# Kernel optimization log

Measured on AMD Instinct MI355X. Metric: run time of the kernel, lower is better.

The kernel has to match this reference:

```python
import jax, jax.numpy as jnp
import numpy as np

EMB_DIM = 4096
INNER = 1024
VOCAB = 32000
NPRED = 3
B, N = 2, 512
EPS = 1e-6
# weighting constants from MLPSpeculator.__init__
STATE_W = 0.5 ** (0.5 / NPRED)
ALPHA = float(np.sqrt((1.0 - STATE_W ** 2) * (INNER / 2.0)) / STATE_W)  # emb_weight / state_weight


def _ln(x, w, b):
    # LayerNormParameterized with use_mean=False (fms default): RMS-style norm + scale + shift
    x = x * jax.lax.rsqrt(jnp.mean(x * x, axis=-1, keepdims=True) + EPS)
    return x * w + b


def setup_inputs() -> dict:
    key = jax.random.key(0)
    ks = jax.random.split(key, 8)
    s = 1.0 / np.sqrt(INNER)  # reset_parameters init scale
    return {
        "state": jax.random.normal(ks[0], (B, N, EMB_DIM), jnp.float32),
        "inds": jax.random.randint(ks[1], (B, N + NPRED), 0, VOCAB, dtype=jnp.int32),
        "emb_w": jax.random.normal(ks[2], (NPRED, VOCAB, INNER), jnp.float32) * s,
        "proj0_w": jax.random.normal(ks[3], (INNER, EMB_DIM), jnp.float32) * s,
        "proj_w": jax.random.normal(ks[4], (NPRED - 1, INNER, INNER), jnp.float32) * s,
        "head_w": jax.random.normal(ks[5], (NPRED, VOCAB, INNER), jnp.float32) * s,
        "ln_w": jnp.ones((NPRED, INNER), jnp.float32),
        "ln_b": jnp.zeros((NPRED, INNER), jnp.float32),
    }


def reference(state, inds, emb_w, proj0_w, proj_w, head_w, ln_w, ln_b):
    n = state.shape[1]
    outs = []
    for i in range(NPRED):
        z = emb_w[i][inds[:, i:i + n]]                      # [b, n, inner] gather
        W = proj0_w if i == 0 else proj_w[i - 1]            # [inner, emb_dim] or [inner, inner]
        state = jnp.einsum('bnd,id->bni', state, W)
        state = state + ALPHA * z                           # torch.add(..., alpha=emb_w/state_w)
        state = jax.nn.gelu(_ln(state, ln_w[i], ln_b[i]), approximate=False)
        outs.append(jnp.einsum('bni,vi->bnv', state, head_w[i]))  # logits [b, n, vocab]
    return jnp.stack(outs, axis=0)                          # [n_predict, b, n, vocab]
```

## Files before the change

### kernel.cpp

```cpp
#include <hip/hip_runtime.h>
#include <hip/hip_bf16.h>
#include <math.h>

#define EMB_DIM 4096
#define INNER   1024
#define VOCAB   32000
#define NPRED   3
#define SEQ     512
#define TOKENS  1024

typedef __attribute__((ext_vector_type(8))) short bf16x8;
typedef __attribute__((ext_vector_type(4))) float f32x4;

__device__ inline void gload_lds16(const void* g, void* l) {
  __builtin_amdgcn_global_load_lds(
      (const __attribute__((address_space(1))) void*)g,
      (__attribute__((address_space(3))) void*)l, 16, 0, 0);
}

__device__ inline unsigned short f2bf(float f) {
  unsigned u = __float_as_uint(f);
  u += 0x7fffu + ((u >> 16) & 1u);
  return (unsigned short)(u >> 16);
}

__global__ void cvt_kernel(const float4* __restrict__ in, ushort4* __restrict__ out, int n4) {
  int stride = gridDim.x * blockDim.x;
  for (int i = blockIdx.x * blockDim.x + threadIdx.x; i < n4; i += stride) {
    float4 v = in[i];
    ushort4 o;
    o.x = f2bf(v.x); o.y = f2bf(v.y); o.z = f2bf(v.z); o.w = f2bf(v.w);
    out[i] = o;
  }
}

__global__ __launch_bounds__(256) void proj_cvt(const __hip_bfloat16* __restrict__ A,
                                                const __hip_bfloat16* __restrict__ Bw,
                                                float* __restrict__ C, int K,
                                                const float4* __restrict__ cvsrc,
                                                ushort4* __restrict__ cvdst, int n4) {
  if (blockIdx.x >= 64) {
    for (int i = (blockIdx.x - 64) * 256 + threadIdx.x; i < n4; i += 960 * 256) {
      float4 v = cvsrc[i];
      ushort4 o;
      o.x = f2bf(v.x); o.y = f2bf(v.y); o.z = f2bf(v.z); o.w = f2bf(v.w);
      cvdst[i] = o;
    }
    return;
  }
  __shared__ char smem[16384];
  char* As = smem;
  char* Bs = smem + 8192;

  const int tid  = threadIdx.x;
  const int lane = tid & 63;
  const int wave = tid >> 6;
  const int wm = wave >> 1, wn = wave & 1;

  const int bm = (blockIdx.x >> 3) * 128;
  const int bn = (blockIdx.x & 7) * 128;
  const int N = 1024;

  const char* Ag = (const char*)(A  + (size_t)(bm + (tid >> 2)) * K + (tid & 3) * 8);
  const char* Bg = (const char*)(Bw + (size_t)(bn + (tid >> 2)) * K + (tid & 3) * 8);
  const size_t rowskip = (size_t)64 * K * 2;

  f32x4 acc[4][4] = {};

  const int fa = (wm * 64 + (lane & 15)) * 64 + (lane >> 4) * 16;
  const int fb = (wn * 64 + (lane & 15)) * 64 + (lane >> 4) * 16;

  for (int k0 = 0; k0 < K; k0 += 32) {
    gload_lds16(Ag,           As + tid * 16);
    gload_lds16(Ag + rowskip, As + 4096 + tid * 16);
    gload_lds16(Bg,           Bs + tid * 16);
    gload_lds16(Bg + rowskip, Bs + 4096 + tid * 16);
    Ag += 64; Bg += 64;
    __syncthreads();

    bf16x8 af[4], bfv[4];
#pragma unroll
    for (int m = 0; m < 4; ++m) af[m]  = *(const bf16x8*)(As + fa + m * 1024);
#pragma unroll
    for (int n = 0; n < 4; ++n) bfv[n] = *(const bf16x8*)(Bs + fb + n * 1024);
#pragma unroll
    for (int m = 0; m < 4; ++m)
#pragma unroll
      for (int n = 0; n < 4; ++n)
        acc[m][n] = __builtin_amdgcn_mfma_f32_16x16x32_bf16(af[m], bfv[n], acc[m][n], 0, 0, 0);
    __syncthreads();
  }

  const int r0 = bm + wm * 64 + (lane >> 4) * 4;
  const int c0 = bn + wn * 64 + (lane & 15);
#pragma unroll
  for (int m = 0; m < 4; ++m)
#pragma unroll
    for (int n = 0; n < 4; ++n) {
      float* Cp = C + (size_t)(r0 + m * 16) * N + (c0 + n * 16);
#pragma unroll
      for (int r = 0; r < 4; ++r)
        Cp[(size_t)r * N] = acc[m][n][r];
    }
}

__global__ __launch_bounds__(512, 2) void mega(const __hip_bfloat16* __restrict__ A,
                                               const __hip_bfloat16* __restrict__ B,
                                               float* __restrict__ C,
                                               const __hip_bfloat16* __restrict__ Pw,
                                               float* __restrict__ nsf,
                                               const float4* __restrict__ cvsrc,
                                               ushort4* __restrict__ cvdst, int n4,
                                               int mode) {
  __shared__ char smem[131072];
  const int tid  = threadIdx.x;
  const int lane = tid & 63;
  const int wave = tid >> 6;

  if (mode == 0 && blockIdx.x >= 564) {
    for (int i = (blockIdx.x - 564) * 512 + tid; i < n4; i += 460 * 512) {
      float4 v = cvsrc[i];
      ushort4 o;
      o.x = f2bf(v.x); o.y = f2bf(v.y); o.z = f2bf(v.z); o.w = f2bf(v.w);
      cvdst[i] = o;
    }
    return;
  }

  if (mode == 0 && blockIdx.x >= 500) {
    char* As = smem;
    char* Bs = smem + 8192;
    const int p = blockIdx.x - 500;
    const int bm = (p >> 3) * 128;
    const int bn = (p & 7) * 128;
    const int wm = wave >> 2, wn = wave & 3;

    const char* Ag = (const char*)(A  + (size_t)(bm + (tid >> 2)) * INNER + (tid & 3) * 8);
    const char* Bg = (const char*)(Pw + (size_t)(bn + (tid >> 2)) * INNER + (tid & 3) * 8);

    f32x4 acc[4][2] = {};
    const int fa = (wm * 64 + (lane & 15)) * 64 + (lane >> 4) * 16;
    const int fb = (wn * 32 + (lane & 15)) * 64 + (lane >> 4) * 16;

    for (int k0 = 0; k0 < INNER; k0 += 32) {
      gload_lds16(Ag, As + tid * 16);
      gload_lds16(Bg, Bs + tid * 16);
      Ag += 64; Bg += 64;
      __syncthreads();
      bf16x8 af[4], bfv[2];
#pragma unroll
      for (int m = 0; m < 4; ++m) af[m]  = *(const bf16x8*)(As + fa + m * 1024);
#pragma unroll
      for (int n = 0; n < 2; ++n) bfv[n] = *(const bf16x8*)(Bs + fb + n * 1024);
#pragma unroll
      for (int m = 0; m < 4; ++m)
#pragma unroll
        for (int n = 0; n < 2; ++n)
          acc[m][n] = __builtin_amdgcn_mfma_f32_16x16x32_bf16(af[m], bfv[n], acc[m][n], 0, 0, 0);
      __syncthreads();
    }
    const int r0 = bm + wm * 64 + (lane >> 4) * 4;
    const int c0 = bn + wn * 32 + (lane & 15);
#pragma unroll
    for (int m = 0; m < 4; ++m)
#pragma unroll
      for (int n = 0; n < 2; ++n) {
        float* Cp = nsf + (size_t)(r0 + m * 16) * INNER + (c0 + n * 16);
#pragma unroll
        for (int r = 0; r < 4; ++r)
          Cp[(size_t)r * INNER] = acc[m][n][r];
      }
    return;
  }

  const int hid = blockIdx.x;
  const int M = TOKENS, N = VOCAB, K = INNER;
  const int wm = wave >> 2;
  const int wn = wave & 3;

  const int MT = M >> 8;
  const int q = 500 >> 3, r = 500 & 7;
  const int xcd = hid & 7, idx = hid >> 3;
  const int wg = (xcd < r ? xcd * (q + 1) : r * (q + 1) + (xcd - r) * q) + idx;
  const int bm = (wg % MT) * 256;
  const int bn = (wg / MT) * 256;

  f32x4 acc[8][4] = {};

  const int sl   = (lane >> 4) ^ ((lane >> 1) & 3);
  const int aoff = (wm * 128 + (lane & 15)) * 64 + sl * 16;
  const int boff = (wn * 64  + (lane & 15)) * 64 + sl * 16;

#define STAGE_T(PTR, BASEROW, LDSBASE, KT_)                                     \
  {                                                                             \
    _Pragma("unroll")                                                           \
    for (int c = 0; c < 2; ++c) {                                               \
      int chunk = c * 512 + tid;                                                \
      int row = chunk >> 2;                                                     \
      int s = (chunk & 3) ^ ((row >> 1) & 3);                                   \
      gload_lds16(PTR + (size_t)((BASEROW) + row) * K + (KT_) * 32 + s * 8,     \
                  smem + (LDSBASE) + chunk * 16);                               \
    }                                                                           \
  }

  STAGE_T(A, bm, 0,             0)
  STAGE_T(B, bn, 65536,         0)
  STAGE_T(A, bm, 16384,         1)
  STAGE_T(B, bn, 65536 + 16384, 1)
  STAGE_T(A, bm, 32768,         2)
  STAGE_T(B, bn, 65536 + 32768, 2)

  const int KT = K >> 5;
  for (int t = 0; t < KT; ++t) {
    const int bc = (t & 3) * 16384;
    const int bs = ((t + 3) & 3) * 16384;
    const char* Ab = smem + bc;
    const char* Bb = smem + 65536 + bc;

    asm volatile("s_waitcnt vmcnt(8)" ::: "memory");
    __builtin_amdgcn_s_barrier();

    const int pk = (t + 3 < KT) ? t + 3 : KT - 1;

    bf16x8 af0[4], bfv[4];
#pragma unroll
    for (int m = 0; m < 4; ++m) af0[m] = *(const bf16x8*)(Ab + aoff + m * 1024);
#pragma unroll
    for (int n = 0; n < 4; ++n) bfv[n] = *(const bf16x8*)(Bb + boff + n * 1024);
    STAGE_T(A, bm, bs, pk)
    asm volatile("s_waitcnt lgkmcnt(0)" ::: "memory");
    __builtin_amdgcn_sched_barrier(0);
    __builtin_amdgcn_s_setprio(1);
#pragma unroll
    for (int m = 0; m < 4; ++m)
#pragma unroll
      for (int n = 0; n < 4; ++n)
        acc[m][n] = __builtin_amdgcn_mfma_f32_16x16x32_bf16(af0[m], bfv[n], acc[m][n], 0, 0, 0);
    __builtin_amdgcn_s_setprio(0);

    bf16x8 af1[4];
#pragma unroll
    for (int m = 0; m < 4; ++m) af1[m] = *(const bf16x8*)(Ab + aoff + (m + 4) * 1024);
    STAGE_T(B, bn, 65536 + bs, pk)
    asm volatile("s_waitcnt lgkmcnt(0)" ::: "memory");
    __builtin_amdgcn_sched_barrier(0);
    __builtin_amdgcn_s_setprio(1);
#pragma unroll
    for (int m = 0; m < 4; ++m)
#pragma unroll
      for (int n = 0; n < 4; ++n)
        acc[m + 4][n] = __builtin_amdgcn_mfma_f32_16x16x32_bf16(af1[m], bfv[n], acc[m + 4][n], 0, 0, 0);
    __builtin_amdgcn_s_setprio(0);
    __builtin_amdgcn_sched_barrier(0);
  }
  asm volatile("s_waitcnt vmcnt(0)" ::: "memory");

  const int r0 = bm + wm * 128 + (lane >> 4) * 4;
  const int c0 = bn + wn * 64 + (lane & 15);
#pragma unroll
  for (int m = 0; m < 8; ++m)
#pragma unroll
    for (int n = 0; n < 4; ++n) {
      float* Cp = C + (size_t)(r0 + m * 16) * N + (c0 + n * 16);
#pragma unroll
      for (int rr = 0; rr < 4; ++rr)
        Cp[(size_t)rr * N] = acc[m][n][rr];
    }
#undef STAGE_T
}

__global__ __launch_bounds__(256) void fuse_ln_gelu(const float* __restrict__ ns,
    const float* __restrict__ emb,
    const int* __restrict__ inds,
    const float* __restrict__ lnw, const float* __restrict__ lnb,
    ushort4* __restrict__ out_bf16,
    int i, float alpha)
{
  const int t = blockIdx.x;
  const int b = t >> 9, n = t & 511;
  const int idx = inds[b * (SEQ + NPRED) + n + i];

  const float4* x = (const float4*)(ns + (size_t)t * INNER);
  const float4* z = (const float4*)(emb + (size_t)idx * INNER);
  const int j = threadIdx.x;

  float4 xv = x[j], zv = z[j];
  float4 v;
  v.x = xv.x + alpha * zv.x;
  v.y = xv.y + alpha * zv.y;
  v.z = xv.z + alpha * zv.z;
  v.w = xv.w + alpha * zv.w;

  float ss = v.x * v.x + v.y * v.y + v.z * v.z + v.w * v.w;
#pragma unroll
  for (int o = 32; o > 0; o >>= 1) ss += __shfl_down(ss, o);
  __shared__ float red[4];
  if ((threadIdx.x & 63) == 0) red[threadIdx.x >> 6] = ss;
  __syncthreads();
  float total = red[0] + red[1] + red[2] + red[3];
  float r = rsqrtf(total * (1.0f / INNER) + 1e-6f);

  float4 wv = ((const float4*)lnw)[j];
  float4 bv = ((const float4*)lnb)[j];
  const float inv_sqrt2 = 0.70710678118654752f;
  ushort4 o;
  float y;
  y = v.x * r * wv.x + bv.x; o.x = f2bf(0.5f * y * (1.0f + erff(y * inv_sqrt2)));
  y = v.y * r * wv.y + bv.y; o.y = f2bf(0.5f * y * (1.0f + erff(y * inv_sqrt2)));
  y = v.z * r * wv.z + bv.z; o.z = f2bf(0.5f * y * (1.0f + erff(y * inv_sqrt2)));
  y = v.w * r * wv.w + bv.w; o.w = f2bf(0.5f * y * (1.0f + erff(y * inv_sqrt2)));

  out_bf16[(size_t)t * (INNER / 4) + j] = o;
}

extern "C" void kernel_launch(void* const* d_in, const int* in_sizes, int n_in,
                              void* d_out, int out_size, void* d_ws, size_t ws_size,
                              hipStream_t stream) {
  const float* state = (const float*)d_in[0];
  const int*   inds  = (const int*)d_in[1];
  const float* emb_w = (const float*)d_in[2];
  const float* proj0 = (const float*)d_in[3];
  const float* projw = (const float*)d_in[4];
  const float* headw = (const float*)d_in[5];
  const float* lnw   = (const float*)d_in[6];
  const float* lnb   = (const float*)d_in[7];
  float* out = (float*)d_out;

  char* ws = (char*)d_ws;
  __hip_bfloat16* stateA = (__hip_bfloat16*)(ws);
  __hip_bfloat16* stateI = (__hip_bfloat16*)(ws + 8388608);
  float*          nsf    = (float*)        (ws + 10485760);
  __hip_bfloat16* p0b    = (__hip_bfloat16*)(ws + 14680064);
  __hip_bfloat16* pwb    = (__hip_bfloat16*)(ws + 23068672);
  __hip_bfloat16* hb0    = (__hip_bfloat16*)(ws + 27262976);
  __hip_bfloat16* hb1    = (__hip_bfloat16*)(ws + 92798976);

  double sw = pow(0.5, 1.0 / 6.0);
  float alpha = (float)(sqrt((1.0 - sw * sw) * (INNER / 2.0)) / sw);

  auto cvt = [&](const float* src, __hip_bfloat16* dst, size_t n) {
    int n4 = (int)(n / 4);
    int blocks = (n4 + 255) / 256;
    if (blocks > 2048) blocks = 2048;
    cvt_kernel<<<dim3(blocks), dim3(256), 0, stream>>>((const float4*)src, (ushort4*)dst, n4);
  };

  const int hn4 = (int)((size_t)VOCAB * INNER / 4);

  cvt(state, stateA, (size_t)TOKENS * EMB_DIM);
  cvt(proj0, p0b, (size_t)INNER * EMB_DIM);
  cvt(projw, pwb, (size_t)2 * INNER * INNER);

  proj_cvt<<<dim3(1024), dim3(256), 0, stream>>>(stateA, p0b, nsf, EMB_DIM,
      (const float4*)headw, (ushort4*)hb0, hn4);
  fuse_ln_gelu<<<dim3(TOKENS), dim3(256), 0, stream>>>(nsf,
      emb_w, inds, lnw, lnb, (ushort4*)stateI, 0, alpha);

  mega<<<dim3(1024), dim3(512), 0, stream>>>(stateI, hb0, out,
      pwb, nsf,
      (const float4*)(headw + (size_t)1 * VOCAB * INNER), (ushort4*)hb1, hn4, 0);
  fuse_ln_gelu<<<dim3(TOKENS), dim3(256), 0, stream>>>(nsf,
      emb_w + (size_t)1 * VOCAB * INNER, inds,
      lnw + INNER, lnb + INNER, (ushort4*)stateI, 1, alpha);

  mega<<<dim3(1024), dim3(512), 0, stream>>>(stateI, hb1, out + (size_t)TOKENS * VOCAB,
      pwb + (size_t)INNER * INNER, nsf,
      (const float4*)(headw + (size_t)2 * VOCAB * INNER), (ushort4*)hb0, hn4, 0);
  fuse_ln_gelu<<<dim3(TOKENS), dim3(256), 0, stream>>>(nsf,
      emb_w + (size_t)2 * VOCAB * INNER, inds,
      lnw + 2 * INNER, lnb + 2 * INNER, (ushort4*)stateI, 2, alpha);

  mega<<<dim3(500), dim3(512), 0, stream>>>(stateI, hb0, out + (size_t)2 * TOKENS * VOCAB,
      pwb, nsf, (const float4*)headw, (ushort4*)hb1, hn4, 1);
}
```

Baseline: 442.4 us.

## Shrink head GEMM tiles to 256x128 with double buffering for higher occupancy

The vocab-head GEMM tile drops from 256x256 to 256x128, and the 4-stage LDS ring becomes a 2-stage double buffer. LDS falls from 128KB to 48KB, which allows 4 workgroups per CU instead of 2, and the grid doubles to 1000 GEMM blocks. The projection GEMM in proj_cvt also moves to 128x64 tiles with 128 blocks, to spread that work over more CUs. The cost is less data reuse per tile, an extra barrier in each k-iteration, and a shallower prefetch depth, so global-load latency is less hidden.

```diff
diff --git a/kernel.cpp b/kernel.cpp
--- a/kernel.cpp
+++ b/kernel.cpp
@@ -39,8 +39,8 @@
                                                 float* __restrict__ C, int K,
                                                 const float4* __restrict__ cvsrc,
                                                 ushort4* __restrict__ cvdst, int n4) {
-  if (blockIdx.x >= 64) {
-    for (int i = (blockIdx.x - 64) * 256 + threadIdx.x; i < n4; i += 960 * 256) {
+  if (blockIdx.x >= 128) {
+    for (int i = (blockIdx.x - 128) * 256 + threadIdx.x; i < n4; i += 896 * 256) {
       float4 v = cvsrc[i];
       ushort4 o;
       o.x = f2bf(v.x); o.y = f2bf(v.y); o.z = f2bf(v.z); o.w = f2bf(v.w);
@@ -48,7 +48,7 @@
     }
     return;
   }
-  __shared__ char smem[16384];
+  __shared__ char smem[12288];
   char* As = smem;
   char* Bs = smem + 8192;
 
@@ -57,46 +57,45 @@
   const int wave = tid >> 6;
   const int wm = wave >> 1, wn = wave & 1;
 
-  const int bm = (blockIdx.x >> 3) * 128;
-  const int bn = (blockIdx.x & 7) * 128;
+  const int bm = (blockIdx.x >> 4) * 128;
+  const int bn = (blockIdx.x & 15) * 64;
   const int N = 1024;
 
   const char* Ag = (const char*)(A  + (size_t)(bm + (tid >> 2)) * K + (tid & 3) * 8);
   const char* Bg = (const char*)(Bw + (size_t)(bn + (tid >> 2)) * K + (tid & 3) * 8);
-  const size_t rowskip = (size_t)64 * K * 2;
-
-  f32x4 acc[4][4] = {};
+  const size_t rowskipA = (size_t)64 * K * 2;
+
+  f32x4 acc[4][2] = {};
 
   const int fa = (wm * 64 + (lane & 15)) * 64 + (lane >> 4) * 16;
-  const int fb = (wn * 64 + (lane & 15)) * 64 + (lane >> 4) * 16;
+  const int fb = (wn * 32 + (lane & 15)) * 64 + (lane >> 4) * 16;
 
   for (int k0 = 0; k0 < K; k0 += 32) {
-    gload_lds16(Ag,           As + tid * 16);
-    gload_lds16(Ag + rowskip, As + 4096 + tid * 16);
-    gload_lds16(Bg,           Bs + tid * 16);
-    gload_lds16(Bg + rowskip, Bs + 4096 + tid * 16);
+    gload_lds16(Ag,            As + tid * 16);
+    gload_lds16(Ag + rowskipA, As + 4096 + tid * 16);
+    gload_lds16(Bg,            Bs + tid * 16);
     Ag += 64; Bg += 64;
     __syncthreads();
 
-    bf16x8 af[4], bfv[4];
+    bf16x8 af[4], bfv[2];
 #pragma unroll
     for (int m = 0; m < 4; ++m) af[m]  = *(const bf16x8*)(As + fa + m * 1024);
 #pragma unroll
-    for (int n = 0; n < 4; ++n) bfv[n] = *(const bf16x8*)(Bs + fb + n * 1024);
+    for (int n = 0; n < 2; ++n) bfv[n] = *(const bf16x8*)(Bs + fb + n * 1024);
 #pragma unroll
     for (int m = 0; m < 4; ++m)
 #pragma unroll
-      for (int n = 0; n < 4; ++n)
+      for (int n = 0; n < 2; ++n)
         acc[m][n] = __builtin_amdgcn_mfma_f32_16x16x32_bf16(af[m], bfv[n], acc[m][n], 0, 0, 0);
     __syncthreads();
   }
 
   const int r0 = bm + wm * 64 + (lane >> 4) * 4;
-  const int c0 = bn + wn * 64 + (lane & 15);
+  const int c0 = bn + wn * 32 + (lane & 15);
 #pragma unroll
   for (int m = 0; m < 4; ++m)
 #pragma unroll
-    for (int n = 0; n < 4; ++n) {
+    for (int n = 0; n < 2; ++n) {
       float* Cp = C + (size_t)(r0 + m * 16) * N + (c0 + n * 16);
 #pragma unroll
       for (int r = 0; r < 4; ++r)
@@ -104,7 +103,7 @@
     }
 }
 
-__global__ __launch_bounds__(512, 2) void mega(const __hip_bfloat16* __restrict__ A,
+__global__ __launch_bounds__(512, 4) void mega(const __hip_bfloat16* __restrict__ A,
                                                const __hip_bfloat16* __restrict__ B,
                                                float* __restrict__ C,
                                                const __hip_bfloat16* __restrict__ Pw,
@@ -112,13 +111,13 @@
                                                const float4* __restrict__ cvsrc,
                                                ushort4* __restrict__ cvdst, int n4,
                                                int mode) {
-  __shared__ char smem[131072];
+  __shared__ char smem[49152];
   const int tid  = threadIdx.x;
   const int lane = tid & 63;
   const int wave = tid >> 6;
 
-  if (mode == 0 && blockIdx.x >= 564) {
-    for (int i = (blockIdx.x - 564) * 512 + tid; i < n4; i += 460 * 512) {
+  if (mode == 0 && blockIdx.x >= 1064) {
+    for (int i = (blockIdx.x - 1064) * 512 + tid; i < n4; i += 460 * 512) {
       float4 v = cvsrc[i];
       ushort4 o;
       o.x = f2bf(v.x); o.y = f2bf(v.y); o.z = f2bf(v.z); o.w = f2bf(v.w);
@@ -127,10 +126,10 @@
     return;
   }
 
-  if (mode == 0 && blockIdx.x >= 500) {
+  if (mode == 0 && blockIdx.x >= 1000) {
     char* As = smem;
     char* Bs = smem + 8192;
-    const int p = blockIdx.x - 500;
+    const int p = blockIdx.x - 1000;
     const int bm = (p >> 3) * 128;
     const int bn = (p & 7) * 128;
     const int wm = wave >> 2, wn = wave & 3;
@@ -174,91 +173,77 @@
   }
 
   const int hid = blockIdx.x;
-  const int M = TOKENS, N = VOCAB, K = INNER;
-  const int wm = wave >> 2;
-  const int wn = wave & 3;
-
-  const int MT = M >> 8;
-  const int q = 500 >> 3, r = 500 & 7;
-  const int xcd = hid & 7, idx = hid >> 3;
-  const int wg = (xcd < r ? xcd * (q + 1) : r * (q + 1) + (xcd - r) * q) + idx;
-  const int bm = (wg % MT) * 256;
-  const int bn = (wg / MT) * 256;
-
-  f32x4 acc[8][4] = {};
+  const int K = INNER, N = VOCAB;
+  const int wm = wave >> 1;
+  const int wn = wave & 1;
+
+  const int wg = (hid & 7) * 125 + (hid >> 3);
+  const int bm = (wg & 3) * 256;
+  const int bn = (wg >> 2) * 128;
+
+  f32x4 acc[4][4] = {};
 
   const int sl   = (lane >> 4) ^ ((lane >> 1) & 3);
-  const int aoff = (wm * 128 + (lane & 15)) * 64 + sl * 16;
-  const int boff = (wn * 64  + (lane & 15)) * 64 + sl * 16;
-
-#define STAGE_T(PTR, BASEROW, LDSBASE, KT_)                                     \
+  const int aoff = (wm * 64 + (lane & 15)) * 64 + sl * 16;
+  const int boff = (wn * 64 + (lane & 15)) * 64 + sl * 16;
+
+#define STAGE_AB(KT_, BUF_)                                                     \
   {                                                                             \
     _Pragma("unroll")                                                           \
     for (int c = 0; c < 2; ++c) {                                               \
       int chunk = c * 512 + tid;                                                \
       int row = chunk >> 2;                                                     \
       int s = (chunk & 3) ^ ((row >> 1) & 3);                                   \
-      gload_lds16(PTR + (size_t)((BASEROW) + row) * K + (KT_) * 32 + s * 8,     \
-                  smem + (LDSBASE) + chunk * 16);                               \
+      gload_lds16(A + (size_t)(bm + row) * K + (KT_) * 32 + s * 8,              \
+                  smem + (BUF_) * 16384 + chunk * 16);                          \
     }                                                                           \
-  }
-
-  STAGE_T(A, bm, 0,             0)
-  STAGE_T(B, bn, 65536,         0)
-  STAGE_T(A, bm, 16384,         1)
-  STAGE_T(B, bn, 65536 + 16384, 1)
-  STAGE_T(A, bm, 32768,         2)
-  STAGE_T(B, bn, 65536 + 32768, 2)
+    {                                                                           \
+      int row = tid >> 2;                                                       \
+      int s = (tid & 3) ^ ((row >> 1) & 3);                                     \
+      gload_lds16(B + (size_t)(bn + row) * K + (KT_) * 32 + s * 8,              \
+                  smem + 32768 + (BUF_) * 8192 + tid * 16);                     \
+    }                                                                           \
+  }
+
+  STAGE_AB(0, 0)
+  STAGE_AB(1, 1)
 
   const int KT = K >> 5;
   for (int t = 0; t < KT; ++t) {
-    const int bc = (t & 3) * 16384;
-    const int bs = ((t + 3) & 3) * 16384;
-    const char* Ab = smem + bc;
-    const char* Bb = smem + 65536 + bc;
-
-    asm volatile("s_waitcnt vmcnt(8)" ::: "memory");
+    const int b = t & 1;
+    const char* Ab = smem + b * 16384;
+    const char* Bb = smem + 32768 + b * 8192;
+
+    asm volatile("s_waitcnt vmcnt(3)" ::: "memory");
     __builtin_amdgcn_s_barrier();
 
-    const int pk = (t + 3 < KT) ? t + 3 : KT - 1;
-
-    bf16x8 af0[4], bfv[4];
-#pragma unroll
-    for (int m = 0; m < 4; ++m) af0[m] = *(const bf16x8*)(Ab + aoff + m * 1024);
+    bf16x8 af[4], bfv[4];
+#pragma unroll
+    for (int m = 0; m < 4; ++m) af[m]  = *(const bf16x8*)(Ab + aoff + m * 1024);
 #pragma unroll
     for (int n = 0; n < 4; ++n) bfv[n] = *(const bf16x8*)(Bb + boff + n * 1024);
-    STAGE_T(A, bm, bs, pk)
     asm volatile("s_waitcnt lgkmcnt(0)" ::: "memory");
     __builtin_amdgcn_sched_barrier(0);
+    __builtin_amdgcn_s_barrier();
+
+    const int pk = (t + 2 < KT) ? t + 2 : KT - 1;
+    STAGE_AB(pk, b)
+
     __builtin_amdgcn_s_setprio(1);
 #pragma unroll
     for (int m = 0; m < 4; ++m)
 #pragma unroll
       for (int n = 0; n < 4; ++n)
-        acc[m][n] = __builtin_amdgcn_mfma_f32_16x16x32_bf16(af0[m], bfv[n], acc[m][n], 0, 0, 0);
-    __builtin_amdgcn_s_setprio(0);
-
-    bf16x8 af1[4];
-#pragma unroll
-    for (int m = 0; m < 4; ++m) af1[m] = *(const bf16x8*)(Ab + aoff + (m + 4) * 1024);
-    STAGE_T(B, bn, 65536 + bs, pk)
-    asm volatile("s_waitcnt lgkmcnt(0)" ::: "memory");
-    __builtin_amdgcn_sched_barrier(0);
-    __builtin_amdgcn_s_setprio(1);
-#pragma unroll
-    for (int m = 0; m < 4; ++m)
-#pragma unroll
-      for (int n = 0; n < 4; ++n)
-        acc[m + 4][n] = __builtin_amdgcn_mfma_f32_16x16x32_bf16(af1[m], bfv[n], acc[m + 4][n], 0, 0, 0);
+        acc[m][n] = __builtin_amdgcn_mfma_f32_16x16x32_bf16(af[m], bfv[n], acc[m][n], 0, 0, 0);
     __builtin_amdgcn_s_setprio(0);
     __builtin_amdgcn_sched_barrier(0);
   }
   asm volatile("s_waitcnt vmcnt(0)" ::: "memory");
 
-  const int r0 = bm + wm * 128 + (lane >> 4) * 4;
+  const int r0 = bm + wm * 64 + (lane >> 4) * 4;
   const int c0 = bn + wn * 64 + (lane & 15);
 #pragma unroll
-  for (int m = 0; m < 8; ++m)
+  for (int m = 0; m < 4; ++m)
 #pragma unroll
     for (int n = 0; n < 4; ++n) {
       float* Cp = C + (size_t)(r0 + m * 16) * N + (c0 + n * 16);
@@ -266,7 +251,7 @@
       for (int rr = 0; rr < 4; ++rr)
         Cp[(size_t)rr * N] = acc[m][n][rr];
     }
-#undef STAGE_T
+#undef STAGE_AB
 }
 
 __global__ __launch_bounds__(256) void fuse_ln_gelu(const float* __restrict__ ns,
@@ -356,20 +341,20 @@
   fuse_ln_gelu<<<dim3(TOKENS), dim3(256), 0, stream>>>(nsf,
       emb_w, inds, lnw, lnb, (ushort4*)stateI, 0, alpha);
 
-  mega<<<dim3(1024), dim3(512), 0, stream>>>(stateI, hb0, out,
+  mega<<<dim3(1524), dim3(512), 0, stream>>>(stateI, hb0, out,
       pwb, nsf,
       (const float4*)(headw + (size_t)1 * VOCAB * INNER), (ushort4*)hb1, hn4, 0);
   fuse_ln_gelu<<<dim3(TOKENS), dim3(256), 0, stream>>>(nsf,
       emb_w + (size_t)1 * VOCAB * INNER, inds,
       lnw + INNER, lnb + INNER, (ushort4*)stateI, 1, alpha);
 
-  mega<<<dim3(1024), dim3(512), 0, stream>>>(stateI, hb1, out + (size_t)TOKENS * VOCAB,
+  mega<<<dim3(1524), dim3(512), 0, stream>>>(stateI, hb1, out + (size_t)TOKENS * VOCAB,
       pwb + (size_t)INNER * INNER, nsf,
       (const float4*)(headw + (size_t)2 * VOCAB * INNER), (ushort4*)hb0, hn4, 0);
   fuse_ln_gelu<<<dim3(TOKENS), dim3(256), 0, stream>>>(nsf,
       emb_w + (size_t)2 * VOCAB * INNER, inds,
       lnw + 2 * INNER, lnb + 2 * INNER, (ushort4*)stateI, 2, alpha);
 
-  mega<<<dim3(500), dim3(512), 0, stream>>>(stateI, hb0, out + (size_t)2 * TOKENS * VOCAB,
+  mega<<<dim3(1000), dim3(512), 0, stream>>>(stateI, hb0, out + (size_t)2 * TOKENS * VOCAB,
       pwb, nsf, (const float4*)headw, (ushort4*)hb1, hn4, 1);
 }
```

Measured after the change: 455.9 us. +3.0%, slower.

## Fuse fp32-to-bf16 conversion of state and proj0 into first projection GEMM

Applied to the files above, without the earlier changes.

Removes the three standalone conversion kernels. The first projection GEMM now reads fp32 state and proj0 directly and rounds them to bf16 in registers before writing to LDS. Its tile changes from 128x128 to 128x64, giving 128 GEMM blocks instead of 64. The proj_w conversion moves onto 8 spare blocks of the same launch, next to the head-weight conversion. This saves launches and the intermediate bf16 round trip, but the GEMM now loads twice the bytes per element through registers instead of direct-to-LDS loads, and proj0 is re-read and re-converted by every row tile.

```diff
diff --git a/kernel.cpp b/kernel.cpp
--- a/kernel.cpp
+++ b/kernel.cpp
@@ -24,31 +24,33 @@
   return (unsigned short)(u >> 16);
 }
 
-__global__ void cvt_kernel(const float4* __restrict__ in, ushort4* __restrict__ out, int n4) {
-  int stride = gridDim.x * blockDim.x;
-  for (int i = blockIdx.x * blockDim.x + threadIdx.x; i < n4; i += stride) {
-    float4 v = in[i];
-    ushort4 o;
-    o.x = f2bf(v.x); o.y = f2bf(v.y); o.z = f2bf(v.z); o.w = f2bf(v.w);
-    out[i] = o;
-  }
-}
-
-__global__ __launch_bounds__(256) void proj_cvt(const __hip_bfloat16* __restrict__ A,
-                                                const __hip_bfloat16* __restrict__ Bw,
-                                                float* __restrict__ C, int K,
-                                                const float4* __restrict__ cvsrc,
-                                                ushort4* __restrict__ cvdst, int n4) {
-  if (blockIdx.x >= 64) {
-    for (int i = (blockIdx.x - 64) * 256 + threadIdx.x; i < n4; i += 960 * 256) {
-      float4 v = cvsrc[i];
+__global__ __launch_bounds__(256) void step0(const float* __restrict__ state,
+                                             const float* __restrict__ p0w,
+                                             float* __restrict__ C,
+                                             const float4* __restrict__ pwsrc,
+                                             ushort4* __restrict__ pwdst, int pn4,
+                                             const float4* __restrict__ hwsrc,
+                                             ushort4* __restrict__ hwdst, int hn4) {
+  if (blockIdx.x >= 136) {
+    for (int i = (blockIdx.x - 136) * 256 + threadIdx.x; i < hn4; i += 888 * 256) {
+      float4 v = hwsrc[i];
       ushort4 o;
       o.x = f2bf(v.x); o.y = f2bf(v.y); o.z = f2bf(v.z); o.w = f2bf(v.w);
-      cvdst[i] = o;
+      hwdst[i] = o;
     }
     return;
   }
-  __shared__ char smem[16384];
+  if (blockIdx.x >= 128) {
+    for (int i = (blockIdx.x - 128) * 256 + threadIdx.x; i < pn4; i += 8 * 256) {
+      float4 v = pwsrc[i];
+      ushort4 o;
+      o.x = f2bf(v.x); o.y = f2bf(v.y); o.z = f2bf(v.z); o.w = f2bf(v.w);
+      pwdst[i] = o;
+    }
+    return;
+  }
+
+  __shared__ char smem[12288];
   char* As = smem;
   char* Bs = smem + 8192;
 
@@ -57,46 +59,60 @@
   const int wave = tid >> 6;
   const int wm = wave >> 1, wn = wave & 1;
 
-  const int bm = (blockIdx.x >> 3) * 128;
-  const int bn = (blockIdx.x & 7) * 128;
+  const int bm = (blockIdx.x >> 4) * 128;
+  const int bn = (blockIdx.x & 15) * 64;
   const int N = 1024;
-
-  const char* Ag = (const char*)(A  + (size_t)(bm + (tid >> 2)) * K + (tid & 3) * 8);
-  const char* Bg = (const char*)(Bw + (size_t)(bn + (tid >> 2)) * K + (tid & 3) * 8);
-  const size_t rowskip = (size_t)64 * K * 2;
-
-  f32x4 acc[4][4] = {};
+  const int K = EMB_DIM;
+
+  const float* Ag = state + (size_t)(bm + (tid >> 2)) * K + (tid & 3) * 8;
+  const float* Bg = p0w   + (size_t)(bn + (tid >> 2)) * K + (tid & 3) * 8;
+  const size_t rowskipA = (size_t)64 * K;
+
+  f32x4 acc[4][2] = {};
 
   const int fa = (wm * 64 + (lane & 15)) * 64 + (lane >> 4) * 16;
-  const int fb = (wn * 64 + (lane & 15)) * 64 + (lane >> 4) * 16;
+  const int fb = (wn * 32 + (lane & 15)) * 64 + (lane >> 4) * 16;
 
   for (int k0 = 0; k0 < K; k0 += 32) {
-    gload_lds16(Ag,           As + tid * 16);
-    gload_lds16(Ag + rowskip, As + 4096 + tid * 16);
-    gload_lds16(Bg,           Bs + tid * 16);
-    gload_lds16(Bg + rowskip, Bs + 4096 + tid * 16);
-    Ag += 64; Bg += 64;
+    {
+      float4 a0 = *(const float4*)(Ag);
+      float4 a1 = *(const float4*)(Ag + 4);
+      float4 a2 = *(const float4*)(Ag + rowskipA);
+      float4 a3 = *(const float4*)(Ag + rowskipA + 4);
+      float4 b0 = *(const float4*)(Bg);
+      float4 b1 = *(const float4*)(Bg + 4);
+      Ag += 32; Bg += 32;
+      ushort s0[8] = { f2bf(a0.x), f2bf(a0.y), f2bf(a0.z), f2bf(a0.w),
+                       f2bf(a1.x), f2bf(a1.y), f2bf(a1.z), f2bf(a1.w) };
+      ushort s1[8] = { f2bf(a2.x), f2bf(a2.y), f2bf(a2.z), f2bf(a2.w),
+                       f2bf(a3.x), f2bf(a3.y), f2bf(a3.z), f2bf(a3.w) };
+      ushort s2[8] = { f2bf(b0.x), f2bf(b0.y), f2bf(b0.z), f2bf(b0.w),
+                       f2bf(b1.x), f2bf(b1.y), f2bf(b1.z), f2bf(b1.w) };
+      *(bf16x8*)(As + tid * 16)        = *(const bf16x8*)s0;
+      *(bf16x8*)(As + 4096 + tid * 16) = *(const bf16x8*)s1;
+      *(bf16x8*)(Bs + tid * 16)        = *(const bf16x8*)s2;
+    }
     __syncthreads();
 
-    bf16x8 af[4], bfv[4];
+    bf16x8 af[4], bfv[2];
 #pragma unroll
     for (int m = 0; m < 4; ++m) af[m]  = *(const bf16x8*)(As + fa + m * 1024);
 #pragma unroll
-    for (int n = 0; n < 4; ++n) bfv[n] = *(const bf16x8*)(Bs + fb + n * 1024);
+    for (int n = 0; n < 2; ++n) bfv[n] = *(const bf16x8*)(Bs + fb + n * 1024);
 #pragma unroll
     for (int m = 0; m < 4; ++m)
 #pragma unroll
-      for (int n = 0; n < 4; ++n)
+      for (int n = 0; n < 2; ++n)
         acc[m][n] = __builtin_amdgcn_mfma_f32_16x16x32_bf16(af[m], bfv[n], acc[m][n], 0, 0, 0);
     __syncthreads();
   }
 
   const int r0 = bm + wm * 64 + (lane >> 4) * 4;
-  const int c0 = bn + wn * 64 + (lane & 15);
+  const int c0 = bn + wn * 32 + (lane & 15);
 #pragma unroll
   for (int m = 0; m < 4; ++m)
 #pragma unroll
-    for (int n = 0; n < 4; ++n) {
+    for (int n = 0; n < 2; ++n) {
       float* Cp = C + (size_t)(r0 + m * 16) * N + (c0 + n * 16);
 #pragma unroll
       for (int r = 0; r < 4; ++r)
@@ -327,31 +343,20 @@
   float* out = (float*)d_out;
 
   char* ws = (char*)d_ws;
-  __hip_bfloat16* stateA = (__hip_bfloat16*)(ws);
-  __hip_bfloat16* stateI = (__hip_bfloat16*)(ws + 8388608);
-  float*          nsf    = (float*)        (ws + 10485760);
-  __hip_bfloat16* p0b    = (__hip_bfloat16*)(ws + 14680064);
-  __hip_bfloat16* pwb    = (__hip_bfloat16*)(ws + 23068672);
-  __hip_bfloat16* hb0    = (__hip_bfloat16*)(ws + 27262976);
-  __hip_bfloat16* hb1    = (__hip_bfloat16*)(ws + 92798976);
+  __hip_bfloat16* stateI = (__hip_bfloat16*)(ws);
+  float*          nsf    = (float*)        (ws + 2097152);
+  __hip_bfloat16* pwb    = (__hip_bfloat16*)(ws + 6291456);
+  __hip_bfloat16* hb0    = (__hip_bfloat16*)(ws + 10485760);
+  __hip_bfloat16* hb1    = (__hip_bfloat16*)(ws + 76021760);
 
   double sw = pow(0.5, 1.0 / 6.0);
   float alpha = (float)(sqrt((1.0 - sw * sw) * (INNER / 2.0)) / sw);
 
-  auto cvt = [&](const float* src, __hip_bfloat16* dst, size_t n) {
-    int n4 = (int)(n / 4);
-    int blocks = (n4 + 255) / 256;
-    if (blocks > 2048) blocks = 2048;
-    cvt_kernel<<<dim3(blocks), dim3(256), 0, stream>>>((const float4*)src, (ushort4*)dst, n4);
-  };
-
   const int hn4 = (int)((size_t)VOCAB * INNER / 4);
-
-  cvt(state, stateA, (size_t)TOKENS * EMB_DIM);
-  cvt(proj0, p0b, (size_t)INNER * EMB_DIM);
-  cvt(projw, pwb, (size_t)2 * INNER * INNER);
-
-  proj_cvt<<<dim3(1024), dim3(256), 0, stream>>>(stateA, p0b, nsf, EMB_DIM,
+  const int pn4 = (int)((size_t)2 * INNER * INNER / 4);
+
+  step0<<<dim3(1024), dim3(256), 0, stream>>>(state, proj0, nsf,
+      (const float4*)projw, (ushort4*)pwb, pn4,
       (const float4*)headw, (ushort4*)hb0, hn4);
   fuse_ln_gelu<<<dim3(TOKENS), dim3(256), 0, stream>>>(nsf,
       emb_w, inds, lnw, lnb, (ushort4*)stateI, 0, alpha);
```

Result: slower. 476.3 us (+7.7%).

## Retile head GEMM into full-M by 64-column blocks with A read from global

Applied to the files above, without the earlier changes.

Restructures the vocab-projection GEMM so each workgroup covers all 1024 tokens and a 64-column slice of the vocabulary. Only the B tile is staged in LDS, double-buffered at K=64 per step. Each wave loads its 128 rows of A straight from global memory into registers. LDS shrinks from 128 KB to 16 KB to allow higher occupancy, but A is now re-read from L2 by every workgroup with no prefetch, which exposes load latency and greatly raises cache traffic.

```diff
diff --git a/kernel.cpp b/kernel.cpp
--- a/kernel.cpp
+++ b/kernel.cpp
@@ -112,7 +112,7 @@
                                                const float4* __restrict__ cvsrc,
                                                ushort4* __restrict__ cvdst, int n4,
                                                int mode) {
-  __shared__ char smem[131072];
+  __shared__ char smem[16384];
   const int tid  = threadIdx.x;
   const int lane = tid & 63;
   const int wave = tid >> 6;
@@ -174,99 +174,76 @@
   }
 
   const int hid = blockIdx.x;
-  const int M = TOKENS, N = VOCAB, K = INNER;
-  const int wm = wave >> 2;
-  const int wn = wave & 3;
-
-  const int MT = M >> 8;
+  const int K = INNER, N = VOCAB;
+
   const int q = 500 >> 3, r = 500 & 7;
   const int xcd = hid & 7, idx = hid >> 3;
   const int wg = (xcd < r ? xcd * (q + 1) : r * (q + 1) + (xcd - r) * q) + idx;
-  const int bm = (wg % MT) * 256;
-  const int bn = (wg / MT) * 256;
+  const int bn = wg * 64;
+
+  const int wavebase = wave * 128;
 
   f32x4 acc[8][4] = {};
 
-  const int sl   = (lane >> 4) ^ ((lane >> 1) & 3);
-  const int aoff = (wm * 128 + (lane & 15)) * 64 + sl * 16;
-  const int boff = (wn * 64  + (lane & 15)) * 64 + sl * 16;
-
-#define STAGE_T(PTR, BASEROW, LDSBASE, KT_)                                     \
+#define STAGE_B(T_, BUF_)                                                       \
   {                                                                             \
-    _Pragma("unroll")                                                           \
-    for (int c = 0; c < 2; ++c) {                                               \
-      int chunk = c * 512 + tid;                                                \
-      int row = chunk >> 2;                                                     \
-      int s = (chunk & 3) ^ ((row >> 1) & 3);                                   \
-      gload_lds16(PTR + (size_t)((BASEROW) + row) * K + (KT_) * 32 + s * 8,     \
-                  smem + (LDSBASE) + chunk * 16);                               \
-    }                                                                           \
-  }
-
-  STAGE_T(A, bm, 0,             0)
-  STAGE_T(B, bn, 65536,         0)
-  STAGE_T(A, bm, 16384,         1)
-  STAGE_T(B, bn, 65536 + 16384, 1)
-  STAGE_T(A, bm, 32768,         2)
-  STAGE_T(B, bn, 65536 + 32768, 2)
-
-  const int KT = K >> 5;
+    int row = tid >> 3;                                                         \
+    int s = (tid & 7) ^ (row & 7);                                              \
+    gload_lds16(B + (size_t)(bn + row) * K + (T_) * 64 + s * 8,                 \
+                smem + (BUF_) * 8192 + tid * 16);                               \
+  }
+
+  STAGE_B(0, 0)
+  STAGE_B(1, 1)
+
+  const int KT = K >> 6;
   for (int t = 0; t < KT; ++t) {
-    const int bc = (t & 3) * 16384;
-    const int bs = ((t + 3) & 3) * 16384;
-    const char* Ab = smem + bc;
-    const char* Bb = smem + 65536 + bc;
-
-    asm volatile("s_waitcnt vmcnt(8)" ::: "memory");
+    const int buf = t & 1;
+
+    if (t < KT - 1) {
+      asm volatile("s_waitcnt vmcnt(1)" ::: "memory");
+    } else {
+      asm volatile("s_waitcnt vmcnt(0)" ::: "memory");
+    }
     __builtin_amdgcn_s_barrier();
 
-    const int pk = (t + 3 < KT) ? t + 3 : KT - 1;
-
-    bf16x8 af0[4], bfv[4];
-#pragma unroll
-    for (int m = 0; m < 4; ++m) af0[m] = *(const bf16x8*)(Ab + aoff + m * 1024);
-#pragma unroll
-    for (int n = 0; n < 4; ++n) bfv[n] = *(const bf16x8*)(Bb + boff + n * 1024);
-    STAGE_T(A, bm, bs, pk)
-    asm volatile("s_waitcnt lgkmcnt(0)" ::: "memory");
-    __builtin_amdgcn_sched_barrier(0);
-    __builtin_amdgcn_s_setprio(1);
-#pragma unroll
-    for (int m = 0; m < 4; ++m)
-#pragma unroll
-      for (int n = 0; n < 4; ++n)
-        acc[m][n] = __builtin_amdgcn_mfma_f32_16x16x32_bf16(af0[m], bfv[n], acc[m][n], 0, 0, 0);
-    __builtin_amdgcn_s_setprio(0);
-
-    bf16x8 af1[4];
-#pragma unroll
-    for (int m = 0; m < 4; ++m) af1[m] = *(const bf16x8*)(Ab + aoff + (m + 4) * 1024);
-    STAGE_T(B, bn, 65536 + bs, pk)
-    asm volatile("s_waitcnt lgkmcnt(0)" ::: "memory");
-    __builtin_amdgcn_sched_barrier(0);
-    __builtin_amdgcn_s_setprio(1);
-#pragma unroll
-    for (int m = 0; m < 4; ++m)
-#pragma unroll
-      for (int n = 0; n < 4; ++n)
-        acc[m + 4][n] = __builtin_amdgcn_mfma_f32_16x16x32_bf16(af1[m], bfv[n], acc[m + 4][n], 0, 0, 0);
-    __builtin_amdgcn_s_setprio(0);
-    __builtin_amdgcn_sched_barrier(0);
-  }
-  asm volatile("s_waitcnt vmcnt(0)" ::: "memory");
-
-  const int r0 = bm + wm * 128 + (lane >> 4) * 4;
-  const int c0 = bn + wn * 64 + (lane & 15);
-#pragma unroll
-  for (int m = 0; m < 8; ++m)
+#pragma unroll
+    for (int kh = 0; kh < 2; ++kh) {
+      bf16x8 af[8], bfv[4];
+#pragma unroll
+      for (int n = 0; n < 4; ++n) {
+        int brow = n * 16 + (lane & 15);
+        int bs = ((kh << 2) + (lane >> 4)) ^ (lane & 7);
+        bfv[n] = *(const bf16x8*)(smem + buf * 8192 + brow * 128 + bs * 16);
+      }
+#pragma unroll
+      for (int m = 0; m < 8; ++m)
+        af[m] = *(const bf16x8*)(A + (size_t)(wavebase + m * 16 + (lane & 15)) * K
+                                   + t * 64 + kh * 32 + (lane >> 4) * 8);
+#pragma unroll
+      for (int m = 0; m < 8; ++m)
+#pragma unroll
+        for (int n = 0; n < 4; ++n)
+          acc[m][n] = __builtin_amdgcn_mfma_f32_16x16x32_bf16(af[m], bfv[n], acc[m][n], 0, 0, 0);
+    }
+
+    __builtin_amdgcn_s_barrier();
+    if (t + 2 < KT) STAGE_B(t + 2, buf)
+  }
+
+  const int c0 = bn + (lane & 15);
+#pragma unroll
+  for (int m = 0; m < 8; ++m) {
+    const int r0 = wavebase + m * 16 + (lane >> 4) * 4;
 #pragma unroll
     for (int n = 0; n < 4; ++n) {
-      float* Cp = C + (size_t)(r0 + m * 16) * N + (c0 + n * 16);
+      float* Cp = C + (size_t)r0 * N + (c0 + n * 16);
 #pragma unroll
       for (int rr = 0; rr < 4; ++rr)
         Cp[(size_t)rr * N] = acc[m][n][rr];
     }
-#undef STAGE_T
+  }
+#undef STAGE_B
 }
 
 __global__ __launch_bounds__(256) void fuse_ln_gelu(const float* __restrict__ ns,
```

Result: slower. 702.9 us (+58.9%).
